# Kernel optimization log

Measured on AMD Instinct MI355X. Metric: run time of the kernel, lower is better.

The kernel has to match this reference:

```python
import jax, jax.numpy as jnp
import numpy as np

B, T, C, H = 2, 2048, 1024, 16
HD = C // H  # head dim = 64


def setup_inputs() -> dict:
    key = jax.random.key(0)
    k1, k2, k3 = jax.random.split(key, 3)
    x = jax.random.normal(k1, (B, T, C), dtype=jnp.float32)
    W_attn = jax.random.normal(k2, (C, 3 * C), dtype=jnp.float32) * (C ** -0.5)
    W_proj = jax.random.normal(k3, (C, C), dtype=jnp.float32) * (C ** -0.5)
    b_proj = jnp.zeros((C,), dtype=jnp.float32)
    return {"x": x, "W_attn": W_attn, "W_proj": W_proj, "b_proj": b_proj}


def reference(x, W_attn, W_proj, b_proj):
    Bv, Tv, Cv = x.shape
    qkv = x @ W_attn  # [B, T, 3C]  (no bias: config.bias=False)
    # NOTE: source splits as k, q, v (k first!)
    k, q, v = jnp.split(qkv, 3, axis=2)
    # [B, H, T, HD]
    q = q.reshape(Bv, Tv, H, HD).transpose(0, 2, 1, 3)
    k = k.reshape(Bv, Tv, H, HD).transpose(0, 2, 1, 3)
    v = v.reshape(Bv, Tv, H, HD).transpose(0, 2, 1, 3)
    wei = jnp.einsum('bhqd,bhkd->bhqk', q, k) * (HD ** -0.5)
    causal = jnp.tril(jnp.ones((Tv, Tv), dtype=bool))
    wei = jnp.where(causal, wei, -jnp.inf)
    wei = jax.nn.softmax(wei, axis=-1)
    # dropout = 0.0 (eval) -> identity
    out = jnp.einsum('bhqk,bhkd->bhqd', wei, v)
    out = out.transpose(0, 2, 1, 3).reshape(Bv, Tv, Cv)
    out = out @ W_proj + b_proj
    return out
```

## Files before the change

### kernel.cpp

```cpp
#include <hip/hip_runtime.h>

typedef __attribute__((ext_vector_type(8))) short short8;
typedef __attribute__((ext_vector_type(4))) short short4v;
typedef __attribute__((ext_vector_type(4))) float float4v;

#define T_SEQ 2048
#define CDIM 1024
#define NHEAD 16
#define HDIM 64

__device__ __forceinline__ unsigned short f2bf(float f) {
    unsigned u = __builtin_bit_cast(unsigned, f);
    u += 0x7FFF + ((u >> 16) & 1);
    return (unsigned short)(u >> 16);
}

__device__ __forceinline__ void gld16(const void* g, void* l) {
    __builtin_amdgcn_global_load_lds(
        (const __attribute__((address_space(1))) void*)g,
        (__attribute__((address_space(3))) void*)l, 16, 0, 0);
}

__global__ __launch_bounds__(256) void convert_f32_bf16_vec(
    const float* __restrict__ in, unsigned short* __restrict__ out) {
    int i = blockIdx.x * 256 + threadIdx.x;
    float4 v = ((const float4*)in)[i];
    ushort4 o;
    o.x = f2bf(v.x); o.y = f2bf(v.y); o.z = f2bf(v.z); o.w = f2bf(v.w);
    ((ushort4*)out)[i] = o;
}

__global__ __launch_bounds__(256) void transpose_f32_bf16(
    const float* __restrict__ in, unsigned short* __restrict__ out, int K, int N) {
    __shared__ float tile[32][33];
    int kb = blockIdx.x * 32, nb = blockIdx.y * 32;
    int tx = threadIdx.x & 31, ty = threadIdx.x >> 5;
    for (int r = 0; r < 4; r++)
        tile[ty + r * 8][tx] = in[(size_t)(kb + ty + r * 8) * N + nb + tx];
    __syncthreads();
    for (int r = 0; r < 4; r++)
        out[(size_t)(nb + ty + r * 8) * K + kb + tx] = f2bf(tile[tx][ty + r * 8]);
}

__global__ __launch_bounds__(256) void gemm_qkv(
    const unsigned short* __restrict__ A, const unsigned short* __restrict__ Bt,
    unsigned short* __restrict__ dK, unsigned short* __restrict__ dQ,
    unsigned short* __restrict__ dV) {
    const int K = 1024;
    __shared__ unsigned short sA[128 * 32];
    __shared__ unsigned short sB[128 * 32];
    int tid = threadIdx.x, wave = tid >> 6, lane = tid & 63;
    int quad = lane >> 4, l16 = lane & 15;
    int wm = wave >> 1, wn = wave & 1;
    int blockM = blockIdx.y * 128, blockN = blockIdx.x * 128;
    int rlane = lane >> 2, seg = lane & 3;
    bool swapAB = (blockN >= 2048);

    const unsigned short* gA = A + (size_t)blockM * K;
    const unsigned short* gB = Bt + (size_t)blockN * K;

    float4v acc[4][4] = {};

    for (int kb = 0; kb < K; kb += 32) {
        __syncthreads();
        for (int i = 0; i < 2; i++) {
            int c = wave * 2 + i;
            int row = c * 16 + rlane;
            gld16(gA + (size_t)row * K + kb + seg * 8, (char*)sA + c * 1024);
            gld16(gB + (size_t)row * K + kb + seg * 8, (char*)sB + c * 1024);
        }
        __syncthreads();
        short8 af[4], bf[4];
        for (int i = 0; i < 4; i++)
            af[i] = *(const short8*)(sA + (wm * 64 + i * 16 + l16) * 32 + quad * 8);
        for (int j = 0; j < 4; j++)
            bf[j] = *(const short8*)(sB + (wn * 64 + j * 16 + l16) * 32 + quad * 8);
        if (!swapAB) {
            for (int i = 0; i < 4; i++)
                for (int j = 0; j < 4; j++)
                    acc[i][j] = __builtin_amdgcn_mfma_f32_16x16x32_bf16(
                        af[i], bf[j], acc[i][j], 0, 0, 0);
        } else {
            for (int i = 0; i < 4; i++)
                for (int j = 0; j < 4; j++)
                    acc[i][j] = __builtin_amdgcn_mfma_f32_16x16x32_bf16(
                        bf[j], af[i], acc[i][j], 0, 0, 0);
        }
    }

    if (!swapAB) {
        const float QSCL = 0.18033688011112042f;
        for (int i = 0; i < 4; i++)
            for (int j = 0; j < 4; j++)
                for (int r = 0; r < 4; r++) {
                    int m = blockM + wm * 64 + i * 16 + quad * 4 + r;
                    int n = blockN + wn * 64 + j * 16 + l16;
                    int part = n >> 10, c = n & 1023;
                    int h = c >> 6, d = c & 63;
                    int bb = m >> 11, t = m & 2047;
                    int bh = bb * NHEAD + h;
                    if (part == 0) {
                        dK[(((size_t)bh * T_SEQ + t) << 6) + d] = f2bf(acc[i][j][r]);
                    } else {
                        dQ[(((size_t)bh * T_SEQ + t) << 6) + d] =
                            f2bf(acc[i][j][r] * QSCL);
                    }
                }
    } else {
        for (int i = 0; i < 4; i++)
            for (int j = 0; j < 4; j++)
                for (int r = 0; r < 4; r++) {
                    int n = blockN + wn * 64 + j * 16 + quad * 4 + r;
                    int m = blockM + wm * 64 + i * 16 + l16;
                    int c = n & 1023;
                    int h = c >> 6, d = c & 63;
                    int bb = m >> 11, t = m & 2047;
                    int bh = bb * NHEAD + h;
                    dV[((size_t)bh * HDIM + d) * T_SEQ + t] = f2bf(acc[i][j][r]);
                }
    }
}

__global__ __launch_bounds__(256) void gemm_proj64(
    const unsigned short* __restrict__ A, const unsigned short* __restrict__ Bt,
    const float* __restrict__ bias, float* __restrict__ out) {
    const int K = 1024;
    __shared__ unsigned short sA[64 * 32];
    __shared__ unsigned short sB[64 * 32];
    int tid = threadIdx.x, wave = tid >> 6, lane = tid & 63;
    int quad = lane >> 4, l16 = lane & 15;
    int wm = wave >> 1, wn = wave & 1;
    int blockM = blockIdx.y * 64, blockN = blockIdx.x * 64;
    int rlane = lane >> 2, seg = lane & 3;

    const unsigned short* gA = A + (size_t)blockM * K;
    const unsigned short* gB = Bt + (size_t)blockN * K;

    float4v acc[2][2] = {};

    for (int kb = 0; kb < K; kb += 32) {
        __syncthreads();
        for (int i = 0; i < 2; i++) {
            int c = wave * 2 + i;
            int isB = c >> 2, cc = c & 3;
            const unsigned short* g = (isB ? gB : gA) +
                (size_t)(cc * 16 + rlane) * K + kb + seg * 8;
            char* l = (char*)(isB ? sB : sA) + cc * 1024;
            gld16(g, l);
        }
        __syncthreads();
        short8 af[2], bf[2];
        for (int i = 0; i < 2; i++)
            af[i] = *(const short8*)(sA + (wm * 32 + i * 16 + l16) * 32 + quad * 8);
        for (int j = 0; j < 2; j++)
            bf[j] = *(const short8*)(sB + (wn * 32 + j * 16 + l16) * 32 + quad * 8);
        for (int i = 0; i < 2; i++)
            for (int j = 0; j < 2; j++)
                acc[i][j] = __builtin_amdgcn_mfma_f32_16x16x32_bf16(
                    af[i], bf[j], acc[i][j], 0, 0, 0);
    }

    for (int i = 0; i < 2; i++)
        for (int j = 0; j < 2; j++)
            for (int r = 0; r < 4; r++) {
                int m = blockM + wm * 32 + i * 16 + quad * 4 + r;
                int n = blockN + wn * 32 + j * 16 + l16;
                out[(size_t)m * CDIM + n] = acc[i][j][r] + bias[n];
            }
}

__global__ __launch_bounds__(256) void attn_fwd(
    const unsigned short* __restrict__ Qp, const unsigned short* __restrict__ Kp,
    const unsigned short* __restrict__ Vt, unsigned short* __restrict__ att) {
    __shared__ unsigned short sK[2][64 * 72];
    __shared__ unsigned short sV[2][64 * 72];
    int tid = threadIdx.x, wave = tid >> 6, lane = tid & 63;
    int quad = lane >> 4, l16 = lane & 15;
    int bh = blockIdx.x;
    int bb = bh >> 4, h = bh & 15;
    size_t baseQ = (size_t)bh * T_SEQ * HDIM;
    size_t baseV = (size_t)bh * HDIM * T_SEQ;
    const int NT = T_SEQ / 64;
    int row4 = tid >> 2, seg = tid & 3;

    for (int pass = 0; pass < 2; pass++) {
        int xt = (pass == 0) ? blockIdx.y : (NT - 1 - blockIdx.y);
        int qb = xt * 64;
        int qrow = qb + wave * 16 + l16;

        const unsigned short* qr = Qp + baseQ + (size_t)qrow * HDIM;
        short8 qf0 = *(const short8*)(qr + quad * 8);
        short8 qf1 = *(const short8*)(qr + 32 + quad * 8);

        float4v o[4] = {};
        float lsum = 0.f;
        int nt = xt + 1;

        uint4 ka, kb2, va, vb;
        {
            const unsigned short* gk = Kp + baseQ + (size_t)row4 * HDIM + seg * 16;
            const unsigned short* gv = Vt + baseV + (size_t)row4 * T_SEQ + seg * 16;
            ka = *(const uint4*)gk; kb2 = *(const uint4*)(gk + 8);
            va = *(const uint4*)gv; vb = *(const uint4*)(gv + 8);
        }
        __syncthreads();
        *(uint4*)(sK[0] + row4 * 72 + seg * 16) = ka;
        *(uint4*)(sK[0] + row4 * 72 + seg * 16 + 8) = kb2;
        *(uint4*)(sV[0] + row4 * 72 + seg * 16) = va;
        *(uint4*)(sV[0] + row4 * 72 + seg * 16 + 8) = vb;

        for (int t = 0; t < nt; t++) {
            int cur = t & 1;
            __syncthreads();
            if (t + 1 < nt) {
                const unsigned short* gk =
                    Kp + baseQ + (size_t)((t + 1) * 64 + row4) * HDIM + seg * 16;
                const unsigned short* gv =
                    Vt + baseV + (size_t)row4 * T_SEQ + (t + 1) * 64 + seg * 16;
                ka = *(const uint4*)gk; kb2 = *(const uint4*)(gk + 8);
                va = *(const uint4*)gv; vb = *(const uint4*)(gv + 8);
            }

            const unsigned short* cK = sK[cur];
            const unsigned short* cV = sV[cur];
            float4v s[4];
            for (int sub = 0; sub < 4; sub++) {
                short8 kf0 = *(const short8*)(cK + (sub * 16 + l16) * 72 + quad * 8);
                short8 kf1 =
                    *(const short8*)(cK + (sub * 16 + l16) * 72 + 32 + quad * 8);
                float4v z = {};
                z = __builtin_amdgcn_mfma_f32_16x16x32_bf16(kf0, qf0, z, 0, 0, 0);
                z = __builtin_amdgcn_mfma_f32_16x16x32_bf16(kf1, qf1, z, 0, 0, 0);
                s[sub] = z;
            }

            bool need_mask = (t * 64 + 63) > (qb + wave * 16);
            float p[16];
            for (int sub = 0; sub < 4; sub++)
                for (int r = 0; r < 4; r++) {
                    float v = s[sub][r];
                    if (need_mask) {
                        int kg = t * 64 + sub * 16 + quad * 4 + r;
                        v = (kg <= qrow) ? v : -1e30f;
                    }
                    p[sub * 4 + r] = v;
                }
            unsigned ub[16];
            for (int i = 0; i < 16; i++) {
                float e = exp2f(p[i] - 16.0f);
                unsigned u = __builtin_bit_cast(unsigned, e) & 0xffff0000u;
                ub[i] = u;
                lsum += __builtin_bit_cast(float, u);
            }

            for (int sub = 0; sub < 4; sub++) {
                unsigned lo = __builtin_amdgcn_perm(ub[sub * 4 + 1], ub[sub * 4 + 0],
                                                    0x07060302u);
                unsigned hi = __builtin_amdgcn_perm(ub[sub * 4 + 3], ub[sub * 4 + 2],
                                                    0x07060302u);
                uint2 packed = {lo, hi};
                short4v pf = __builtin_bit_cast(short4v, packed);
                for (int dc = 0; dc < 4; dc++) {
                    short4v vf = *(const short4v*)(
                        cV + (dc * 16 + l16) * 72 + sub * 16 + quad * 4);
                    o[dc] = __builtin_amdgcn_mfma_f32_16x16x16bf16_1k(
                        vf, pf, o[dc], 0, 0, 0);
                }
            }

            if (t + 1 < nt) {
                int nxt = cur ^ 1;
                *(uint4*)(sK[nxt] + row4 * 72 + seg * 16) = ka;
                *(uint4*)(sK[nxt] + row4 * 72 + seg * 16 + 8) = kb2;
                *(uint4*)(sV[nxt] + row4 * 72 + seg * 16) = va;
                *(uint4*)(sV[nxt] + row4 * 72 + seg * 16 + 8) = vb;
            }
        }

        lsum += __shfl_xor(lsum, 16);
        lsum += __shfl_xor(lsum, 32);
        float inv = 1.0f / lsum;

        __syncthreads();
        for (int dc = 0; dc < 4; dc++) {
            short4v ov;
            for (int r = 0; r < 4; r++) ov[r] = (short)f2bf(o[dc][r] * inv);
            *(short4v*)(sK[0] + wave * 1152 + l16 * 72 + dc * 16 + quad * 4) = ov;
        }
        __syncthreads();
        int orow = lane >> 2, oseg = lane & 3;
        uint4 a = *(const uint4*)(sK[0] + wave * 1152 + orow * 72 + oseg * 16);
        uint4 b = *(const uint4*)(sK[0] + wave * 1152 + orow * 72 + oseg * 16 + 8);
        unsigned short* dst = att +
            (size_t)(bb * T_SEQ + qb + wave * 16 + orow) * CDIM + h * HDIM +
            oseg * 16;
        *(uint4*)dst = a;
        *(uint4*)(dst + 8) = b;
    }
}

extern "C" void kernel_launch(void* const* d_in, const int* in_sizes, int n_in,
                              void* d_out, int out_size, void* d_ws, size_t ws_size,
                              hipStream_t stream) {
    const float* x      = (const float*)d_in[0];
    const float* W_attn = (const float*)d_in[1];
    const float* W_proj = (const float*)d_in[2];
    const float* b_proj = (const float*)d_in[3];
    float* out = (float*)d_out;

    unsigned short* xb   = (unsigned short*)d_ws;
    unsigned short* WaT  = xb  + 4096 * 1024;
    unsigned short* WpT  = WaT + 3072 * 1024;
    unsigned short* Karr = WpT + 1024 * 1024;
    unsigned short* Qarr = Karr + 2 * 16 * 2048 * 64;
    unsigned short* Varr = Qarr + 2 * 16 * 2048 * 64;
    unsigned short* attb = Varr + 2 * 16 * 2048 * 64;

    convert_f32_bf16_vec<<<4096, 256, 0, stream>>>(x, xb);
    transpose_f32_bf16<<<dim3(32, 96), 256, 0, stream>>>(W_attn, WaT, 1024, 3072);
    transpose_f32_bf16<<<dim3(32, 32), 256, 0, stream>>>(W_proj, WpT, 1024, 1024);
    gemm_qkv<<<dim3(24, 32), 256, 0, stream>>>(xb, WaT, Karr, Qarr, Varr);
    attn_fwd<<<dim3(32, 16), 256, 0, stream>>>(Qarr, Karr, Varr, attb);
    gemm_proj64<<<dim3(16, 64), 256, 0, stream>>>(attb, WpT, b_proj, out);
}
```

Before: 212.6 us.

## Double-buffer GEMM tiles with register prefetch instead of direct global-to-LDS loads

Both the QKV and projection GEMMs now load the next K-slice into registers while MFMAs run on the current LDS buffer, then store it into a second LDS buffer. This replaces the global_load_lds path and its two barriers per iteration with one barrier and ping-pong buffers, so global latency can overlap compute. It costs extra LDS (double buffers), extra VGPRs for the staged data, and explicit LDS write instructions.

Result: faster. 204.0 us (-4.0%).

```diff
diff --git a/kernel.cpp b/kernel.cpp
--- a/kernel.cpp
+++ b/kernel.cpp
@@ -13,12 +13,6 @@
     unsigned u = __builtin_bit_cast(unsigned, f);
     u += 0x7FFF + ((u >> 16) & 1);
     return (unsigned short)(u >> 16);
-}
-
-__device__ __forceinline__ void gld16(const void* g, void* l) {
-    __builtin_amdgcn_global_load_lds(
-        (const __attribute__((address_space(1))) void*)g,
-        (__attribute__((address_space(3))) void*)l, 16, 0, 0);
 }
 
 __global__ __launch_bounds__(256) void convert_f32_bf16_vec(
@@ -47,8 +41,9 @@
     unsigned short* __restrict__ dK, unsigned short* __restrict__ dQ,
     unsigned short* __restrict__ dV) {
     const int K = 1024;
-    __shared__ unsigned short sA[128 * 32];
-    __shared__ unsigned short sB[128 * 32];
+    const int NITER = K / 32;
+    __shared__ unsigned short sA[2][128 * 32];
+    __shared__ unsigned short sB[2][128 * 32];
     int tid = threadIdx.x, wave = tid >> 6, lane = tid & 63;
     int quad = lane >> 4, l16 = lane & 15;
     int wm = wave >> 1, wn = wave & 1;
@@ -60,21 +55,37 @@
     const unsigned short* gB = Bt + (size_t)blockN * K;
 
     float4v acc[4][4] = {};
-
-    for (int kb = 0; kb < K; kb += 32) {
-        __syncthreads();
-        for (int i = 0; i < 2; i++) {
-            int c = wave * 2 + i;
-            int row = c * 16 + rlane;
-            gld16(gA + (size_t)row * K + kb + seg * 8, (char*)sA + c * 1024);
-            gld16(gB + (size_t)row * K + kb + seg * 8, (char*)sB + c * 1024);
-        }
-        __syncthreads();
+    uint4 ra[2], rb[2];
+
+    for (int i = 0; i < 2; i++) {
+        int row = wave * 32 + i * 16 + rlane;
+        ra[i] = *(const uint4*)(gA + (size_t)row * K + seg * 8);
+        rb[i] = *(const uint4*)(gB + (size_t)row * K + seg * 8);
+    }
+    for (int i = 0; i < 2; i++) {
+        int c = wave * 2 + i;
+        *(uint4*)((char*)sA[0] + c * 1024 + lane * 16) = ra[i];
+        *(uint4*)((char*)sB[0] + c * 1024 + lane * 16) = rb[i];
+    }
+
+    for (int it = 0; it < NITER; it++) {
+        int cur = it & 1;
+        __syncthreads();
+        if (it + 1 < NITER) {
+            int kb = (it + 1) * 32;
+            for (int i = 0; i < 2; i++) {
+                int row = wave * 32 + i * 16 + rlane;
+                ra[i] = *(const uint4*)(gA + (size_t)row * K + kb + seg * 8);
+                rb[i] = *(const uint4*)(gB + (size_t)row * K + kb + seg * 8);
+            }
+        }
+        const unsigned short* cA = sA[cur];
+        const unsigned short* cB = sB[cur];
         short8 af[4], bf[4];
         for (int i = 0; i < 4; i++)
-            af[i] = *(const short8*)(sA + (wm * 64 + i * 16 + l16) * 32 + quad * 8);
+            af[i] = *(const short8*)(cA + (wm * 64 + i * 16 + l16) * 32 + quad * 8);
         for (int j = 0; j < 4; j++)
-            bf[j] = *(const short8*)(sB + (wn * 64 + j * 16 + l16) * 32 + quad * 8);
+            bf[j] = *(const short8*)(cB + (wn * 64 + j * 16 + l16) * 32 + quad * 8);
         if (!swapAB) {
             for (int i = 0; i < 4; i++)
                 for (int j = 0; j < 4; j++)
@@ -85,6 +96,14 @@
                 for (int j = 0; j < 4; j++)
                     acc[i][j] = __builtin_amdgcn_mfma_f32_16x16x32_bf16(
                         bf[j], af[i], acc[i][j], 0, 0, 0);
+        }
+        if (it + 1 < NITER) {
+            int nxt = cur ^ 1;
+            for (int i = 0; i < 2; i++) {
+                int c = wave * 2 + i;
+                *(uint4*)((char*)sA[nxt] + c * 1024 + lane * 16) = ra[i];
+                *(uint4*)((char*)sB[nxt] + c * 1024 + lane * 16) = rb[i];
+            }
         }
     }
 
@@ -125,8 +144,9 @@
     const unsigned short* __restrict__ A, const unsigned short* __restrict__ Bt,
     const float* __restrict__ bias, float* __restrict__ out) {
     const int K = 1024;
-    __shared__ unsigned short sA[64 * 32];
-    __shared__ unsigned short sB[64 * 32];
+    const int NITER = K / 32;
+    __shared__ unsigned short sA[2][64 * 32];
+    __shared__ unsigned short sB[2][64 * 32];
     int tid = threadIdx.x, wave = tid >> 6, lane = tid & 63;
     int quad = lane >> 4, l16 = lane & 15;
     int wm = wave >> 1, wn = wave & 1;
@@ -137,27 +157,52 @@
     const unsigned short* gB = Bt + (size_t)blockN * K;
 
     float4v acc[2][2] = {};
-
-    for (int kb = 0; kb < K; kb += 32) {
-        __syncthreads();
-        for (int i = 0; i < 2; i++) {
-            int c = wave * 2 + i;
-            int isB = c >> 2, cc = c & 3;
-            const unsigned short* g = (isB ? gB : gA) +
-                (size_t)(cc * 16 + rlane) * K + kb + seg * 8;
-            char* l = (char*)(isB ? sB : sA) + cc * 1024;
-            gld16(g, l);
-        }
-        __syncthreads();
+    uint4 r2[2];
+
+    for (int i = 0; i < 2; i++) {
+        int c = wave * 2 + i;
+        int isB = c >> 2, cc = c & 3;
+        r2[i] = *(const uint4*)((isB ? gB : gA) +
+                                (size_t)(cc * 16 + rlane) * K + seg * 8);
+    }
+    for (int i = 0; i < 2; i++) {
+        int c = wave * 2 + i;
+        int isB = c >> 2, cc = c & 3;
+        *(uint4*)((char*)(isB ? sB[0] : sA[0]) + cc * 1024 + lane * 16) = r2[i];
+    }
+
+    for (int it = 0; it < NITER; it++) {
+        int cur = it & 1;
+        __syncthreads();
+        if (it + 1 < NITER) {
+            int kb = (it + 1) * 32;
+            for (int i = 0; i < 2; i++) {
+                int c = wave * 2 + i;
+                int isB = c >> 2, cc = c & 3;
+                r2[i] = *(const uint4*)((isB ? gB : gA) +
+                                        (size_t)(cc * 16 + rlane) * K + kb + seg * 8);
+            }
+        }
+        const unsigned short* cA = sA[cur];
+        const unsigned short* cB = sB[cur];
         short8 af[2], bf[2];
         for (int i = 0; i < 2; i++)
-            af[i] = *(const short8*)(sA + (wm * 32 + i * 16 + l16) * 32 + quad * 8);
+            af[i] = *(const short8*)(cA + (wm * 32 + i * 16 + l16) * 32 + quad * 8);
         for (int j = 0; j < 2; j++)
-            bf[j] = *(const short8*)(sB + (wn * 32 + j * 16 + l16) * 32 + quad * 8);
+            bf[j] = *(const short8*)(cB + (wn * 32 + j * 16 + l16) * 32 + quad * 8);
         for (int i = 0; i < 2; i++)
             for (int j = 0; j < 2; j++)
                 acc[i][j] = __builtin_amdgcn_mfma_f32_16x16x32_bf16(
                     af[i], bf[j], acc[i][j], 0, 0, 0);
+        if (it + 1 < NITER) {
+            int nxt = cur ^ 1;
+            for (int i = 0; i < 2; i++) {
+                int c = wave * 2 + i;
+                int isB = c >> 2, cc = c & 3;
+                *(uint4*)((char*)(isB ? sB[nxt] : sA[nxt]) + cc * 1024 + lane * 16) =
+                    r2[i];
+            }
+        }
     }
 
     for (int i = 0; i < 2; i++)
```
